# Optimization experiments

Measured on AMD Instinct MI355X. Metric: run time of the kernel, lower is better.

## Reference

```python
import jax, jax.numpy as jnp
import numpy as np

S = 7
B = 2
C = 20
LAMBDA_COORD = 5.0
LAMBDA_NOOBJ = 0.5
EPS = 1e-6
N_IMG = 8192
N_GT = 32


def setup_inputs() -> dict:
    key = jax.random.key(0)
    k1, k2, k3 = jax.random.split(key, 3)
    outputs = jax.random.uniform(k1, (N_IMG, S, S, B * 5 + C), dtype=jnp.float32)
    gt_boxes = jax.random.uniform(k2, (N_IMG, N_GT, 4), dtype=jnp.float32)
    gt_labels = jax.random.randint(k3, (N_IMG, N_GT), 0, C)
    return {"outputs": outputs, "gt_boxes": gt_boxes, "gt_labels": gt_labels}


def _pairwise_iou(pred, gt):
    # pred: [N,S,S,B,1,4], gt: [N,1,1,1,G,4], boxes in (cx, cy, w, h) format
    px1 = pred[..., 0] - pred[..., 2] * 0.5
    py1 = pred[..., 1] - pred[..., 3] * 0.5
    px2 = pred[..., 0] + pred[..., 2] * 0.5
    py2 = pred[..., 1] + pred[..., 3] * 0.5
    gx1 = gt[..., 0] - gt[..., 2] * 0.5
    gy1 = gt[..., 1] - gt[..., 3] * 0.5
    gx2 = gt[..., 0] + gt[..., 2] * 0.5
    gy2 = gt[..., 1] + gt[..., 3] * 0.5
    iw = jnp.clip(jnp.minimum(px2, gx2) - jnp.maximum(px1, gx1), 0.0)
    ih = jnp.clip(jnp.minimum(py2, gy2) - jnp.maximum(py1, gy1), 0.0)
    inter = iw * ih
    union = pred[..., 2] * pred[..., 3] + gt[..., 2] * gt[..., 3] - inter
    return inter / (union + EPS)  # [N,S,S,B,G]


def reference(outputs, gt_boxes, gt_labels):
    N = outputs.shape[0]
    pb = outputs[..., : B * 5].reshape(N, S, S, B, 5)
    pbox = pb[..., :4]          # [N,S,S,B,4]
    pconf = pb[..., 4]          # [N,S,S,B]
    pcls = outputs[..., B * 5:] # [N,S,S,C]

    iou = _pairwise_iou(pbox[:, :, :, :, None, :], gt_boxes[:, None, None, None, :, :])
    best_iou = iou.max(axis=-1)      # [N,S,S,B]
    best_idx = iou.argmax(axis=-1)   # [N,S,S,B]

    # gather matched GT boxes: [N,S,S,B,4]
    matched = jnp.take_along_axis(
        gt_boxes[:, None, None, None, :, :], best_idx[..., None, None], axis=4
    ).squeeze(4)

    loc = LAMBDA_COORD * (
        (pbox[..., 0] - matched[..., 0]) ** 2
        + (pbox[..., 1] - matched[..., 1]) ** 2
        + (jnp.sqrt(pbox[..., 2]) - jnp.sqrt(matched[..., 2])) ** 2
        + (jnp.sqrt(pbox[..., 3]) - jnp.sqrt(matched[..., 3])) ** 2
    )
    conf_obj = (pconf - best_iou) ** 2

    # multi-hot class target per image (scatter 1 at every GT label)
    multihot = jnp.zeros((N, C), outputs.dtype).at[
        jnp.arange(N)[:, None], gt_labels
    ].set(1.0)
    # soft-target cross entropy: -sum(t * log_softmax(logits)) per cell
    ce = -(jax.nn.log_softmax(pcls, axis=-1) * multihot[:, None, None, :]).sum(-1)  # [N,S,S]

    has_obj = best_iou > 0.0
    per_box = jnp.where(has_obj, loc + conf_obj + ce[..., None], LAMBDA_NOOBJ * pconf ** 2)
    return per_box.sum() / N
```

## Files before the change

kernel.cpp:

```cpp
#include <hip/hip_runtime.h>
#include <hip/hip_bf16.h>

#define NC 20
#define NCELL 49
#define NGT 32
#define NIMG 8192
#define NTOT (NIMG * NCELL)
#define CPB 128
#define NBLK (NTOT / CPB)
#define NSPAN 4
#define LAMBDA_COORD 5.0f
#define LAMBDA_NOOBJ 0.5f
#define EPS_IOU 1e-6f

__global__ __launch_bounds__(256, 8) void yolo_main_kernel(
    const float* __restrict__ outputs,
    const float* __restrict__ gt_boxes,
    const int*   __restrict__ gt_labels,
    float* __restrict__ partials)
{
    __shared__ float4   s_act4[CPB * 30 / 4];
    __shared__ float4   s_gtc[NSPAN * NGT];
    __shared__ float    s_ga [NSPAN * NGT];
    __shared__ unsigned s_mask[NSPAN];
    __shared__ float    s_w[4];

    const int tid = threadIdx.x;
    const unsigned base   = blockIdx.x * CPB;
    const unsigned img_lo = base / NCELL;
    const unsigned off    = base - img_lo * NCELL;

    if (tid < NSPAN) s_mask[tid] = 0u;
    __syncthreads();

    if (tid < 128) {
        const unsigned g   = tid >> 5;
        const unsigned img = img_lo + g;
        if (img < NIMG) {
            float4 b = reinterpret_cast<const float4*>(gt_boxes)[img * NGT + (tid & 31)];
            s_gtc[tid] = make_float4(fmaf(b.z, -0.5f, b.x), fmaf(b.w, -0.5f, b.y),
                                     fmaf(b.z,  0.5f, b.x), fmaf(b.w,  0.5f, b.y));
            s_ga[tid] = b.z * b.w;
        }
    } else {
        const int t = tid - 128;
        const unsigned g   = t >> 5;
        const unsigned img = img_lo + g;
        if (img < NIMG) {
            int lab = gt_labels[img * NGT + (t & 31)];
            atomicOr(&s_mask[g], 1u << lab);
        }
    }

    const float4* asrc = reinterpret_cast<const float4*>(outputs) + (size_t)base * 30 / 4;
    #pragma unroll
    for (int k = 0; k < 4; ++k) {
        int i = tid + k * 256;
        if (i < CPB * 30 / 4) s_act4[i] = asrc[i];
    }
    __syncthreads();

    const int p = tid & 1;
    const int s = tid >> 1;
    const unsigned rel  = ((unsigned)(s + off) * 1339u) >> 16;
    const unsigned mask = s_mask[rel];
    const float2* a2 = reinterpret_cast<const float2*>(s_act4) + s * 15;

    const float2* cp = a2 + 5 + p * 5;
    float2 c0 = cp[0], c1 = cp[1], c2 = cp[2], c3 = cp[3], c4 = cp[4];
    float mxh = fmaxf(fmaxf(fmaxf(c0.x, c0.y), fmaxf(c1.x, c1.y)),
                      fmaxf(fmaxf(c2.x, c2.y), fmaxf(c3.x, c3.y)));
    mxh = fmaxf(mxh, fmaxf(c4.x, c4.y));
    const unsigned mh = mask >> (p * 10);
    float selh = ((mh & 1u)   ? c0.x : 0.f) + ((mh & 2u)   ? c0.y : 0.f)
               + ((mh & 4u)   ? c1.x : 0.f) + ((mh & 8u)   ? c1.y : 0.f)
               + ((mh & 16u)  ? c2.x : 0.f) + ((mh & 32u)  ? c2.y : 0.f)
               + ((mh & 64u)  ? c3.x : 0.f) + ((mh & 128u) ? c3.y : 0.f)
               + ((mh & 256u) ? c4.x : 0.f) + ((mh & 512u) ? c4.y : 0.f);
    const float mx = fmaxf(mxh, __shfl_xor(mxh, 1));
    float ssh = __expf(c0.x - mx) + __expf(c0.y - mx)
              + __expf(c1.x - mx) + __expf(c1.y - mx)
              + __expf(c2.x - mx) + __expf(c2.y - mx)
              + __expf(c3.x - mx) + __expf(c3.y - mx)
              + __expf(c4.x - mx) + __expf(c4.y - mx);
    const float ssum = ssh + __shfl_xor(ssh, 1);
    const float sel  = selh + __shfl_xor(selh, 1);
    const float ce = (float)__popc(mask) * (mx + __logf(ssum)) - sel;

    float2 A = a2[2 * p], Bv = a2[2 * p + 1], Cv = a2[2 * p + 2];
    const float cx = p ? A.y  : A.x;
    const float cy = p ? Bv.x : A.y;
    const float w  = p ? Bv.y : Bv.x;
    const float h  = p ? Cv.x : Bv.y;
    const float cf = p ? Cv.y : Cv.x;

    const float px1 = fmaf(w, -0.5f, cx), py1 = fmaf(h, -0.5f, cy);
    const float px2 = fmaf(w,  0.5f, cx), py2 = fmaf(h,  0.5f, cy);
    const float pae = w * h + EPS_IOU;

    const float4* gtc = s_gtc + rel * NGT;
    const float*  gab = s_ga  + rel * NGT;
    float bin = -1.f, bS = 1.f;
    int bi = 0;
    #pragma unroll
    for (int j = 0; j < NGT; j += 2) {
        float4 g0 = gtc[j], g1 = gtc[j + 1];
        float2 ar = *reinterpret_cast<const float2*>(gab + j);
        {
            float iw = fmaxf(fminf(px2, g0.z) - fmaxf(px1, g0.x), 0.f);
            float ih = fmaxf(fminf(py2, g0.w) - fmaxf(py1, g0.y), 0.f);
            float in = iw * ih, S = pae + ar.x;
            if (in * bS > bin * S) { bin = in; bS = S; bi = j; }
        }
        {
            float iw = fmaxf(fminf(px2, g1.z) - fmaxf(px1, g1.x), 0.f);
            float ih = fmaxf(fminf(py2, g1.w) - fmaxf(py1, g1.y), 0.f);
            float in = iw * ih, S = pae + ar.y;
            if (in * bS > bin * S) { bin = in; bS = S; bi = j + 1; }
        }
    }

    float term;
    if (bin > 0.f) {
        float4 g = gtc[bi];
        const float iou = __fdividef(bin, bS - bin);
        const float dx = cx - (g.x + g.z) * 0.5f;
        const float dy = cy - (g.y + g.w) * 0.5f;
        const float dw = sqrtf(w) - sqrtf(g.z - g.x);
        const float dh = sqrtf(h) - sqrtf(g.w - g.y);
        term = LAMBDA_COORD * (dx * dx + dy * dy + dw * dw + dh * dh)
             + (cf - iou) * (cf - iou) + ce;
    } else {
        term = LAMBDA_NOOBJ * cf * cf;
    }

    float partial = term;
    #pragma unroll
    for (int o = 32; o > 0; o >>= 1)
        partial += __shfl_down(partial, o);
    if ((tid & 63) == 0) s_w[tid >> 6] = partial;
    __syncthreads();
    if (tid == 0)
        partials[blockIdx.x] = s_w[0] + s_w[1] + s_w[2] + s_w[3];
}

__global__ __launch_bounds__(256) void yolo_reduce_kernel(
    const float* __restrict__ partials, float* __restrict__ out)
{
    float s = 0.f;
    for (int i = threadIdx.x; i < NBLK; i += 256) s += partials[i];
    #pragma unroll
    for (int o = 32; o > 0; o >>= 1)
        s += __shfl_down(s, o);
    __shared__ float s_w[4];
    const int tid = threadIdx.x;
    if ((tid & 63) == 0) s_w[tid >> 6] = s;
    __syncthreads();
    if (tid == 0)
        out[0] = (s_w[0] + s_w[1] + s_w[2] + s_w[3]) * (1.0f / (float)NIMG);
}

extern "C" void kernel_launch(void* const* d_in, const int* in_sizes, int n_in,
                              void* d_out, int out_size, void* d_ws, size_t ws_size,
                              hipStream_t stream) {
    const float* outputs   = (const float*)d_in[0];
    const float* gt_boxes  = (const float*)d_in[1];
    const int*   gt_labels = (const int*)d_in[2];
    float* out      = (float*)d_out;
    float* partials = (float*)d_ws;

    yolo_main_kernel<<<NBLK, 256, 0, stream>>>(outputs, gt_boxes, gt_labels, partials);
    yolo_reduce_kernel<<<1, 256, 0, stream>>>(partials, out);
}
```

Measured before the change: 32.06 us.

## Split GT scan across thread pair, each lane evaluating both predicted boxes

Each pair of threads previously had each lane scan all 32 GT boxes for its own predicted box. Now each lane scans half of the GT boxes (16) for both predicted boxes. The partial argmax results are exchanged with a shuffle and merged using tie-breaking that keeps the first-index semantics. This halves the shared-memory GT loads per thread and uses float4 area loads. The cost is extra registers and a cross-lane merge step.

```diff
diff --git a/kernel.cpp b/kernel.cpp
--- a/kernel.cpp
+++ b/kernel.cpp
@@ -1,5 +1,4 @@
 #include <hip/hip_runtime.h>
-#include <hip/hip_bf16.h>
 
 #define NC 20
 #define NCELL 49
@@ -21,7 +20,7 @@
 {
     __shared__ float4   s_act4[CPB * 30 / 4];
     __shared__ float4   s_gtc[NSPAN * NGT];
-    __shared__ float    s_ga [NSPAN * NGT];
+    __shared__ float4   s_ga4[NSPAN * NGT / 4];
     __shared__ unsigned s_mask[NSPAN];
     __shared__ float    s_w[4];
 
@@ -40,7 +39,7 @@
             float4 b = reinterpret_cast<const float4*>(gt_boxes)[img * NGT + (tid & 31)];
             s_gtc[tid] = make_float4(fmaf(b.z, -0.5f, b.x), fmaf(b.w, -0.5f, b.y),
                                      fmaf(b.z,  0.5f, b.x), fmaf(b.w,  0.5f, b.y));
-            s_ga[tid] = b.z * b.w;
+            reinterpret_cast<float*>(s_ga4)[tid] = b.z * b.w;
         }
     } else {
         const int t = tid - 128;
@@ -87,38 +86,58 @@
     const float sel  = selh + __shfl_xor(selh, 1);
     const float ce = (float)__popc(mask) * (mx + __logf(ssum)) - sel;
 
-    float2 A = a2[2 * p], Bv = a2[2 * p + 1], Cv = a2[2 * p + 2];
-    const float cx = p ? A.y  : A.x;
-    const float cy = p ? Bv.x : A.y;
-    const float w  = p ? Bv.y : Bv.x;
-    const float h  = p ? Cv.x : Bv.y;
-    const float cf = p ? Cv.y : Cv.x;
-
-    const float px1 = fmaf(w, -0.5f, cx), py1 = fmaf(h, -0.5f, cy);
-    const float px2 = fmaf(w,  0.5f, cx), py2 = fmaf(h,  0.5f, cy);
-    const float pae = w * h + EPS_IOU;
+    float2 q0 = a2[0], q1 = a2[1], q2 = a2[2], q3 = a2[3], q4 = a2[4];
+    const float cx0 = q0.x, cy0 = q0.y, w0 = q1.x, h0 = q1.y, cf0 = q2.x;
+    const float cx1 = q2.y, cy1 = q3.x, w1 = q3.y, h1 = q4.x, cf1 = q4.y;
+    const float px1_0 = fmaf(w0, -0.5f, cx0), py1_0 = fmaf(h0, -0.5f, cy0);
+    const float px2_0 = fmaf(w0,  0.5f, cx0), py2_0 = fmaf(h0,  0.5f, cy0);
+    const float px1_1 = fmaf(w1, -0.5f, cx1), py1_1 = fmaf(h1, -0.5f, cy1);
+    const float px2_1 = fmaf(w1,  0.5f, cx1), py2_1 = fmaf(h1,  0.5f, cy1);
+    const float pa0e = w0 * h0 + EPS_IOU, pa1e = w1 * h1 + EPS_IOU;
 
     const float4* gtc = s_gtc + rel * NGT;
-    const float*  gab = s_ga  + rel * NGT;
-    float bin = -1.f, bS = 1.f;
-    int bi = 0;
+    const float4* gmy = gtc + p * 16;
+    const float4* amy = s_ga4 + rel * (NGT / 4) + p * 4;
+    float bin0 = -1.f, bS0 = 1.f, bin1 = -1.f, bS1 = 1.f;
+    int bi0 = 0, bi1 = 0;
     #pragma unroll
-    for (int j = 0; j < NGT; j += 2) {
-        float4 g0 = gtc[j], g1 = gtc[j + 1];
-        float2 ar = *reinterpret_cast<const float2*>(gab + j);
-        {
-            float iw = fmaxf(fminf(px2, g0.z) - fmaxf(px1, g0.x), 0.f);
-            float ih = fmaxf(fminf(py2, g0.w) - fmaxf(py1, g0.y), 0.f);
-            float in = iw * ih, S = pae + ar.x;
-            if (in * bS > bin * S) { bin = in; bS = S; bi = j; }
-        }
-        {
-            float iw = fmaxf(fminf(px2, g1.z) - fmaxf(px1, g1.x), 0.f);
-            float ih = fmaxf(fminf(py2, g1.w) - fmaxf(py1, g1.y), 0.f);
-            float in = iw * ih, S = pae + ar.y;
-            if (in * bS > bin * S) { bin = in; bS = S; bi = j + 1; }
-        }
+    for (int jc = 0; jc < 16; jc += 4) {
+        float4 g0 = gmy[jc], g1 = gmy[jc + 1], g2 = gmy[jc + 2], g3 = gmy[jc + 3];
+        float4 ar = amy[jc >> 2];
+        #define UPD2(g, ga_, j_) do {                                           \
+            float iw0 = fmaxf(fminf(px2_0, (g).z) - fmaxf(px1_0, (g).x), 0.f);  \
+            float ih0 = fmaxf(fminf(py2_0, (g).w) - fmaxf(py1_0, (g).y), 0.f);  \
+            float in0 = iw0 * ih0, S0 = pa0e + (ga_);                           \
+            if (in0 * bS0 > bin0 * S0) { bin0 = in0; bS0 = S0; bi0 = (j_); }    \
+            float iw1 = fmaxf(fminf(px2_1, (g).z) - fmaxf(px1_1, (g).x), 0.f);  \
+            float ih1 = fmaxf(fminf(py2_1, (g).w) - fmaxf(py1_1, (g).y), 0.f);  \
+            float in1 = iw1 * ih1, S1 = pa1e + (ga_);                           \
+            if (in1 * bS1 > bin1 * S1) { bin1 = in1; bS1 = S1; bi1 = (j_); }    \
+        } while (0)
+        UPD2(g0, ar.x, jc);
+        UPD2(g1, ar.y, jc + 1);
+        UPD2(g2, ar.z, jc + 2);
+        UPD2(g3, ar.w, jc + 3);
     }
+
+    const float oin = p ? bin1 : bin0;
+    const float oS  = p ? bS1  : bS0;
+    const int   obi = p * 16 + (p ? bi1 : bi0);
+    const float sin_ = p ? bin0 : bin1;
+    const float sS   = p ? bS0  : bS1;
+    const int   sbi  = p * 16 + (p ? bi0 : bi1);
+    const float rin = __shfl_xor(sin_, 1);
+    const float rS  = __shfl_xor(sS, 1);
+    const int   rbi = __shfl_xor(sbi, 1);
+    const float a_ = rin * oS, b_ = oin * rS;
+    const bool take = p ? (a_ >= b_) : (a_ > b_);
+    const float bin = take ? rin : oin;
+    const float bS  = take ? rS  : oS;
+    const int   bi  = take ? rbi : obi;
+
+    const float cx = p ? cx1 : cx0, cy = p ? cy1 : cy0;
+    const float w  = p ? w1  : w0,  h  = p ? h1  : h0;
+    const float cf = p ? cf1 : cf0;
 
     float term;
     if (bin > 0.f) {
```

After: 33.55 us. +4.6%, slower.

## Make main kernel persistent with double-buffered register-staged tile prefetch

Applied to the files above, without the earlier changes.

Replaces one-block-per-tile launch with 1024 persistent blocks, each looping over 3-4 tiles of 128 cells. The next tile's activations, GT boxes and labels are loaded into registers while the current tile is computed, then written to a second LDS buffer. This is meant to hide global load latency and cut launch and reduction overhead, with the reduce kernel summing only 1024 partials. In exchange it doubles LDS use, raises register pressure (occupancy hint lowered to 4), and adds two barriers per tile.

```diff
diff --git a/kernel.cpp b/kernel.cpp
--- a/kernel.cpp
+++ b/kernel.cpp
@@ -1,5 +1,4 @@
 #include <hip/hip_runtime.h>
-#include <hip/hip_bf16.h>
 
 #define NC 20
 #define NCELL 49
@@ -7,148 +6,188 @@
 #define NIMG 8192
 #define NTOT (NIMG * NCELL)
 #define CPB 128
-#define NBLK (NTOT / CPB)
+#define NTILE (NTOT / CPB)
+#define PBLK 1024
 #define NSPAN 4
 #define LAMBDA_COORD 5.0f
 #define LAMBDA_NOOBJ 0.5f
 #define EPS_IOU 1e-6f
 
-__global__ __launch_bounds__(256, 8) void yolo_main_kernel(
+__global__ __launch_bounds__(256, 4) void yolo_main_kernel(
     const float* __restrict__ outputs,
     const float* __restrict__ gt_boxes,
     const int*   __restrict__ gt_labels,
     float* __restrict__ partials)
 {
-    __shared__ float4   s_act4[CPB * 30 / 4];
-    __shared__ float4   s_gtc[NSPAN * NGT];
-    __shared__ float    s_ga [NSPAN * NGT];
-    __shared__ unsigned s_mask[NSPAN];
+    __shared__ float4   s_act4[2][CPB * 30 / 4];
+    __shared__ float4   s_gtc[2][NSPAN * NGT];
+    __shared__ float    s_ga [2][NSPAN * NGT];
+    __shared__ unsigned s_mask[2][NSPAN];
     __shared__ float    s_w[4];
 
     const int tid = threadIdx.x;
-    const unsigned base   = blockIdx.x * CPB;
-    const unsigned img_lo = base / NCELL;
-    const unsigned off    = base - img_lo * NCELL;
-
-    if (tid < NSPAN) s_mask[tid] = 0u;
-    __syncthreads();
-
-    if (tid < 128) {
-        const unsigned g   = tid >> 5;
-        const unsigned img = img_lo + g;
-        if (img < NIMG) {
-            float4 b = reinterpret_cast<const float4*>(gt_boxes)[img * NGT + (tid & 31)];
-            s_gtc[tid] = make_float4(fmaf(b.z, -0.5f, b.x), fmaf(b.w, -0.5f, b.y),
-                                     fmaf(b.z,  0.5f, b.x), fmaf(b.w,  0.5f, b.y));
-            s_ga[tid] = b.z * b.w;
+    const int bid = blockIdx.x;
+    const int nt  = 3 + (bid < (NTILE - 3 * PBLK) ? 1 : 0);
+
+    float acc = 0.f;
+
+    float4 r0, r1, r2, r3, gtr;
+    int labr = 0;
+    unsigned g_img = NIMG;
+
+#define STAGE_ISSUE(base_, nb_) do {                                          \
+    const float4* asrc_ = reinterpret_cast<const float4*>(outputs)            \
+                        + (size_t)(base_) * 30 / 4;                           \
+    r0 = asrc_[tid];                                                          \
+    r1 = asrc_[tid + 256];                                                    \
+    r2 = asrc_[tid + 512];                                                    \
+    if (tid < 192) r3 = asrc_[tid + 768];                                     \
+    const unsigned il_ = (base_) / NCELL;                                     \
+    if (tid < 128) {                                                          \
+        const unsigned g_ = (unsigned)tid >> 5;                               \
+        g_img = il_ + g_;                                                     \
+        if (g_img < NIMG)                                                     \
+            gtr = reinterpret_cast<const float4*>(gt_boxes)[g_img * NGT + (tid & 31)]; \
+    } else {                                                                  \
+        const int t_ = tid - 128;                                             \
+        const unsigned g_ = (unsigned)t_ >> 5;                                \
+        g_img = il_ + g_;                                                     \
+        if (g_img < NIMG) labr = gt_labels[g_img * NGT + (t_ & 31)];          \
+        if (t_ < NSPAN) s_mask[nb_][t_] = 0u;                                 \
+    }                                                                         \
+} while (0)
+
+#define STAGE_WRITE(nb_) do {                                                 \
+    s_act4[nb_][tid]       = r0;                                              \
+    s_act4[nb_][tid + 256] = r1;                                              \
+    s_act4[nb_][tid + 512] = r2;                                              \
+    if (tid < 192) s_act4[nb_][tid + 768] = r3;                               \
+    if (tid < 128) {                                                          \
+        if (g_img < NIMG) {                                                   \
+            s_gtc[nb_][tid] = make_float4(fmaf(gtr.z, -0.5f, gtr.x),          \
+                                          fmaf(gtr.w, -0.5f, gtr.y),          \
+                                          fmaf(gtr.z,  0.5f, gtr.x),          \
+                                          fmaf(gtr.w,  0.5f, gtr.y));         \
+            s_ga[nb_][tid] = gtr.z * gtr.w;                                   \
+        }                                                                     \
+    } else {                                                                  \
+        const int t_ = tid - 128;                                             \
+        if (g_img < NIMG) atomicOr(&s_mask[nb_][t_ >> 5], 1u << labr);        \
+    }                                                                         \
+} while (0)
+
+    STAGE_ISSUE((unsigned)bid * CPB, 0);
+    __syncthreads();
+    STAGE_WRITE(0);
+    __syncthreads();
+
+    int cur = 0;
+    for (int k = 0; k < nt; ++k) {
+        const unsigned tile = (unsigned)bid + (unsigned)k * PBLK;
+        const unsigned base = tile * CPB;
+        const bool hn = (k + 1 < nt);
+        if (hn) STAGE_ISSUE((tile + PBLK) * CPB, cur ^ 1);
+
+        const unsigned img_lo = base / NCELL;
+        const unsigned off    = base - img_lo * NCELL;
+
+        const int p = tid & 1;
+        const int s = tid >> 1;
+        const unsigned rel  = ((unsigned)(s + off) * 1339u) >> 16;
+        const unsigned mask = s_mask[cur][rel];
+        const float2* a2 = reinterpret_cast<const float2*>(s_act4[cur]) + s * 15;
+
+        const float2* cp = a2 + 5 + p * 5;
+        float2 c0 = cp[0], c1 = cp[1], c2 = cp[2], c3 = cp[3], c4 = cp[4];
+        float mxh = fmaxf(fmaxf(fmaxf(c0.x, c0.y), fmaxf(c1.x, c1.y)),
+                          fmaxf(fmaxf(c2.x, c2.y), fmaxf(c3.x, c3.y)));
+        mxh = fmaxf(mxh, fmaxf(c4.x, c4.y));
+        const unsigned mh = mask >> (p * 10);
+        float selh = ((mh & 1u)   ? c0.x : 0.f) + ((mh & 2u)   ? c0.y : 0.f)
+                   + ((mh & 4u)   ? c1.x : 0.f) + ((mh & 8u)   ? c1.y : 0.f)
+                   + ((mh & 16u)  ? c2.x : 0.f) + ((mh & 32u)  ? c2.y : 0.f)
+                   + ((mh & 64u)  ? c3.x : 0.f) + ((mh & 128u) ? c3.y : 0.f)
+                   + ((mh & 256u) ? c4.x : 0.f) + ((mh & 512u) ? c4.y : 0.f);
+        const float mx = fmaxf(mxh, __shfl_xor(mxh, 1));
+        float ssh = __expf(c0.x - mx) + __expf(c0.y - mx)
+                  + __expf(c1.x - mx) + __expf(c1.y - mx)
+                  + __expf(c2.x - mx) + __expf(c2.y - mx)
+                  + __expf(c3.x - mx) + __expf(c3.y - mx)
+                  + __expf(c4.x - mx) + __expf(c4.y - mx);
+        const float ssum = ssh + __shfl_xor(ssh, 1);
+        const float sel  = selh + __shfl_xor(selh, 1);
+        const float ce = (float)__popc(mask) * (mx + __logf(ssum)) - sel;
+
+        float2 A = a2[2 * p], Bv = a2[2 * p + 1], Cv = a2[2 * p + 2];
+        const float cx = p ? A.y  : A.x;
+        const float cy = p ? Bv.x : A.y;
+        const float w  = p ? Bv.y : Bv.x;
+        const float h  = p ? Cv.x : Bv.y;
+        const float cf = p ? Cv.y : Cv.x;
+
+        const float px1 = fmaf(w, -0.5f, cx), py1 = fmaf(h, -0.5f, cy);
+        const float px2 = fmaf(w,  0.5f, cx), py2 = fmaf(h,  0.5f, cy);
+        const float pae = w * h + EPS_IOU;
+
+        const float4* gtc = s_gtc[cur] + rel * NGT;
+        const float*  gab = s_ga[cur]  + rel * NGT;
+        float bin = -1.f, bS = 1.f;
+        int bi = 0;
+        #pragma unroll
+        for (int j = 0; j < NGT; j += 2) {
+            float4 g0 = gtc[j], g1 = gtc[j + 1];
+            float2 ar = *reinterpret_cast<const float2*>(gab + j);
+            {
+                float iw = fmaxf(fminf(px2, g0.z) - fmaxf(px1, g0.x), 0.f);
+                float ih = fmaxf(fminf(py2, g0.w) - fmaxf(py1, g0.y), 0.f);
+                float in = iw * ih, S = pae + ar.x;
+                if (in * bS > bin * S) { bin = in; bS = S; bi = j; }
+            }
+            {
+                float iw = fmaxf(fminf(px2, g1.z) - fmaxf(px1, g1.x), 0.f);
+                float ih = fmaxf(fminf(py2, g1.w) - fmaxf(py1, g1.y), 0.f);
+                float in = iw * ih, S = pae + ar.y;
+                if (in * bS > bin * S) { bin = in; bS = S; bi = j + 1; }
+            }
         }
-    } else {
-        const int t = tid - 128;
-        const unsigned g   = t >> 5;
-        const unsigned img = img_lo + g;
-        if (img < NIMG) {
-            int lab = gt_labels[img * NGT + (t & 31)];
-            atomicOr(&s_mask[g], 1u << lab);
+
+        float term;
+        if (bin > 0.f) {
+            float4 g = gtc[bi];
+            const float iou = __fdividef(bin, bS - bin);
+            const float dx = cx - (g.x + g.z) * 0.5f;
+            const float dy = cy - (g.y + g.w) * 0.5f;
+            const float dw = sqrtf(w) - sqrtf(g.z - g.x);
+            const float dh = sqrtf(h) - sqrtf(g.w - g.y);
+            term = LAMBDA_COORD * (dx * dx + dy * dy + dw * dw + dh * dh)
+                 + (cf - iou) * (cf - iou) + ce;
+        } else {
+            term = LAMBDA_NOOBJ * cf * cf;
         }
+        acc += term;
+
+        __syncthreads();
+        if (hn) STAGE_WRITE(cur ^ 1);
+        __syncthreads();
+        cur ^= 1;
     }
 
-    const float4* asrc = reinterpret_cast<const float4*>(outputs) + (size_t)base * 30 / 4;
-    #pragma unroll
-    for (int k = 0; k < 4; ++k) {
-        int i = tid + k * 256;
-        if (i < CPB * 30 / 4) s_act4[i] = asrc[i];
-    }
-    __syncthreads();
-
-    const int p = tid & 1;
-    const int s = tid >> 1;
-    const unsigned rel  = ((unsigned)(s + off) * 1339u) >> 16;
-    const unsigned mask = s_mask[rel];
-    const float2* a2 = reinterpret_cast<const float2*>(s_act4) + s * 15;
-
-    const float2* cp = a2 + 5 + p * 5;
-    float2 c0 = cp[0], c1 = cp[1], c2 = cp[2], c3 = cp[3], c4 = cp[4];
-    float mxh = fmaxf(fmaxf(fmaxf(c0.x, c0.y), fmaxf(c1.x, c1.y)),
-                      fmaxf(fmaxf(c2.x, c2.y), fmaxf(c3.x, c3.y)));
-    mxh = fmaxf(mxh, fmaxf(c4.x, c4.y));
-    const unsigned mh = mask >> (p * 10);
-    float selh = ((mh & 1u)   ? c0.x : 0.f) + ((mh & 2u)   ? c0.y : 0.f)
-               + ((mh & 4u)   ? c1.x : 0.f) + ((mh & 8u)   ? c1.y : 0.f)
-               + ((mh & 16u)  ? c2.x : 0.f) + ((mh & 32u)  ? c2.y : 0.f)
-               + ((mh & 64u)  ? c3.x : 0.f) + ((mh & 128u) ? c3.y : 0.f)
-               + ((mh & 256u) ? c4.x : 0.f) + ((mh & 512u) ? c4.y : 0.f);
-    const float mx = fmaxf(mxh, __shfl_xor(mxh, 1));
-    float ssh = __expf(c0.x - mx) + __expf(c0.y - mx)
-              + __expf(c1.x - mx) + __expf(c1.y - mx)
-              + __expf(c2.x - mx) + __expf(c2.y - mx)
-              + __expf(c3.x - mx) + __expf(c3.y - mx)
-              + __expf(c4.x - mx) + __expf(c4.y - mx);
-    const float ssum = ssh + __shfl_xor(ssh, 1);
-    const float sel  = selh + __shfl_xor(selh, 1);
-    const float ce = (float)__popc(mask) * (mx + __logf(ssum)) - sel;
-
-    float2 A = a2[2 * p], Bv = a2[2 * p + 1], Cv = a2[2 * p + 2];
-    const float cx = p ? A.y  : A.x;
-    const float cy = p ? Bv.x : A.y;
-    const float w  = p ? Bv.y : Bv.x;
-    const float h  = p ? Cv.x : Bv.y;
-    const float cf = p ? Cv.y : Cv.x;
-
-    const float px1 = fmaf(w, -0.5f, cx), py1 = fmaf(h, -0.5f, cy);
-    const float px2 = fmaf(w,  0.5f, cx), py2 = fmaf(h,  0.5f, cy);
-    const float pae = w * h + EPS_IOU;
-
-    const float4* gtc = s_gtc + rel * NGT;
-    const float*  gab = s_ga  + rel * NGT;
-    float bin = -1.f, bS = 1.f;
-    int bi = 0;
-    #pragma unroll
-    for (int j = 0; j < NGT; j += 2) {
-        float4 g0 = gtc[j], g1 = gtc[j + 1];
-        float2 ar = *reinterpret_cast<const float2*>(gab + j);
-        {
-            float iw = fmaxf(fminf(px2, g0.z) - fmaxf(px1, g0.x), 0.f);
-            float ih = fmaxf(fminf(py2, g0.w) - fmaxf(py1, g0.y), 0.f);
-            float in = iw * ih, S = pae + ar.x;
-            if (in * bS > bin * S) { bin = in; bS = S; bi = j; }
-        }
-        {
-            float iw = fmaxf(fminf(px2, g1.z) - fmaxf(px1, g1.x), 0.f);
-            float ih = fmaxf(fminf(py2, g1.w) - fmaxf(py1, g1.y), 0.f);
-            float in = iw * ih, S = pae + ar.y;
-            if (in * bS > bin * S) { bin = in; bS = S; bi = j + 1; }
-        }
-    }
-
-    float term;
-    if (bin > 0.f) {
-        float4 g = gtc[bi];
-        const float iou = __fdividef(bin, bS - bin);
-        const float dx = cx - (g.x + g.z) * 0.5f;
-        const float dy = cy - (g.y + g.w) * 0.5f;
-        const float dw = sqrtf(w) - sqrtf(g.z - g.x);
-        const float dh = sqrtf(h) - sqrtf(g.w - g.y);
-        term = LAMBDA_COORD * (dx * dx + dy * dy + dw * dw + dh * dh)
-             + (cf - iou) * (cf - iou) + ce;
-    } else {
-        term = LAMBDA_NOOBJ * cf * cf;
-    }
-
-    float partial = term;
     #pragma unroll
     for (int o = 32; o > 0; o >>= 1)
-        partial += __shfl_down(partial, o);
-    if ((tid & 63) == 0) s_w[tid >> 6] = partial;
+        acc += __shfl_down(acc, o);
+    if ((tid & 63) == 0) s_w[tid >> 6] = acc;
     __syncthreads();
     if (tid == 0)
-        partials[blockIdx.x] = s_w[0] + s_w[1] + s_w[2] + s_w[3];
+        partials[bid] = s_w[0] + s_w[1] + s_w[2] + s_w[3];
 }
 
 __global__ __launch_bounds__(256) void yolo_reduce_kernel(
     const float* __restrict__ partials, float* __restrict__ out)
 {
     float s = 0.f;
-    for (int i = threadIdx.x; i < NBLK; i += 256) s += partials[i];
+    #pragma unroll
+    for (int k = 0; k < PBLK / 256; ++k)
+        s += partials[threadIdx.x + k * 256];
     #pragma unroll
     for (int o = 32; o > 0; o >>= 1)
         s += __shfl_down(s, o);
@@ -169,6 +208,6 @@
     float* out      = (float*)d_out;
     float* partials = (float*)d_ws;
 
-    yolo_main_kernel<<<NBLK, 256, 0, stream>>>(outputs, gt_boxes, gt_labels, partials);
+    yolo_main_kernel<<<PBLK, 256, 0, stream>>>(outputs, gt_boxes, gt_labels, partials);
     yolo_reduce_kernel<<<1, 256, 0, stream>>>(partials, out);
 }
```

Measured after the change: 28.92 us. 1.11x faster.
